# Kernel tuning notes

Measured on AMD Instinct MI355X. Metric: run time of the kernel, lower is better.

The kernel has to match this reference:

```python
import jax, jax.numpy as jnp
import numpy as np

BATCH = 32
NUM_PRIORS = 8732
NUM_CLASSES = 81          # includes background class 0
CENTER_VAR = 0.1
SIZE_VAR = 0.2
CONF_THR = 0.01
NMS_THR = 0.45
TOPK = 100                # per-class NMS candidates
MAX_DET = 100             # max detections per image


def setup_inputs() -> dict:
    key = jax.random.key(0)
    k1, k2, k3 = jax.random.split(key, 3)
    cls_logits = jax.random.normal(k1, (BATCH, NUM_PRIORS, NUM_CLASSES), jnp.float32)
    bbox_pred = jax.random.normal(k2, (BATCH, NUM_PRIORS, 4), jnp.float32)
    # center-form priors (cx, cy, w, h) in (0, 1)
    priors = jax.random.uniform(k3, (NUM_PRIORS, 4), jnp.float32, 0.05, 0.95)
    return {"cls_logits": cls_logits, "bbox_pred": bbox_pred, "priors": priors}


def _decode(loc, priors):
    # convert_locations_to_boxes (center form) then center_form_to_corner_form
    cxcy = loc[..., :2] * CENTER_VAR * priors[..., 2:] + priors[..., :2]
    wh = jnp.exp(loc[..., 2:] * SIZE_VAR) * priors[..., 2:]
    return jnp.concatenate([cxcy - wh * 0.5, cxcy + wh * 0.5], axis=-1)  # [.., 4] xyxy


def _pairwise_iou(b):
    # b: [K, 4] corner form
    lt = jnp.maximum(b[:, None, :2], b[None, :, :2])
    rb = jnp.minimum(b[:, None, 2:], b[None, :, 2:])
    wh = jnp.clip(rb - lt, 0.0)
    inter = wh[..., 0] * wh[..., 1]
    area = jnp.clip(b[:, 2] - b[:, 0], 0.0) * jnp.clip(b[:, 3] - b[:, 1], 0.0)
    return inter / (area[:, None] + area[None, :] - inter + 1e-9)


def _per_class_nms(scores_n, boxes_n):
    # scores_n: [N], boxes_n: [N, 4]
    s, idx = jax.lax.top_k(scores_n, TOPK)
    b = boxes_n[idx]                                # [K, 4]
    iou = _pairwise_iou(b)                          # [K, K]
    init = s > CONF_THR
    rng = jnp.arange(TOPK)

    def body(i, keep):
        sup = (iou[i] > NMS_THR) & keep[i] & (rng > i)
        return keep & ~sup

    keep = jax.lax.fori_loop(0, TOPK, body, init)   # greedy NMS on sorted boxes
    return jnp.where(keep, s, 0.0), b


def reference(cls_logits, bbox_pred, priors):
    scores = jax.nn.softmax(cls_logits, axis=-1)            # [B, N, C]
    boxes = _decode(bbox_pred, priors)                      # [B, N, 4]
    cls_scores = jnp.swapaxes(scores[..., 1:], 1, 2)        # [B, C-1, N] skip background
    nms_fn = jax.vmap(jax.vmap(_per_class_nms, in_axes=(0, None)), in_axes=(0, 0))
    s_k, b_k = nms_fn(cls_scores, boxes)                    # [B, C-1, K], [B, C-1, K, 4]
    labels = jnp.broadcast_to(jnp.arange(1, NUM_CLASSES)[None, :, None], s_k.shape)
    B = s_k.shape[0]
    flat = (NUM_CLASSES - 1) * TOPK
    s_f = s_k.reshape(B, flat)
    b_f = b_k.reshape(B, flat, 4)
    l_f = labels.reshape(B, flat)
    top_s, top_i = jax.lax.top_k(s_f, MAX_DET)              # keep best MAX_DET per image
    top_b = jnp.take_along_axis(b_f, top_i[..., None], axis=1)
    top_l = jnp.take_along_axis(l_f, top_i, axis=1)
    return top_b, top_s, top_l.astype(jnp.int32)
```

## Files before the change

kernel.cpp:

```cpp
#include <hip/hip_runtime.h>
#include <hip/hip_bf16.h>
#include <float.h>

#define BATCH    32
#define NPRIORS  8732
#define NT32     274
#define NPAD     (NT32 * 32)
#define NV4T     (NPAD / 4)
#define NCLASSES 81
#define NC1      80
#define TOPK     100
#define MAXDET   100
#define FLATC    (NC1 * TOPK)
#define FV4      2000
#define NCAND    512
#define NBIN     1024
#define BINOFF   3040

__global__ __launch_bounds__(256, 4) void softmax_transpose_kernel(
    const float* __restrict__ logits, float* __restrict__ scores_t) {
  int b = blockIdx.x / NT32;
  int tile = blockIdx.x - b * NT32;
  int n0 = tile * 32;
  int rows = min(32, NPRIORS - n0);

  int t = threadIdx.x;
  int r = t >> 3;
  int q = t & 7;

  __shared__ __align__(16) float lds[NC1 * 40];

  const bool live = (r < rows);

  float v[11];
  float s = 0.f;
  if (live) {
    const float* rowp = logits + ((size_t)b * NPRIORS + n0 + r) * NCLASSES;
#pragma unroll
    for (int k = 0; k < 10; ++k) v[k] = rowp[q + (k << 3)];
    v[10] = (q == 0) ? rowp[80] : -FLT_MAX;

    float m = -FLT_MAX;
#pragma unroll
    for (int k = 0; k < 10; ++k) m = fmaxf(m, v[k]);
    if (q == 0) m = fmaxf(m, v[10]);
    m = fmaxf(m, __shfl_xor(m, 1));
    m = fmaxf(m, __shfl_xor(m, 2));
    m = fmaxf(m, __shfl_xor(m, 4));

#pragma unroll
    for (int k = 0; k < 10; ++k) {
      v[k] = expf(v[k] - m);
      s += v[k];
    }
    if (q == 0) {
      v[10] = expf(v[10] - m);
      s += v[10];
    }
    s += __shfl_xor(s, 1);
    s += __shfl_xor(s, 2);
    s += __shfl_xor(s, 4);

#pragma unroll
    for (int k = 0; k < 10; ++k) {
      int c = q + (k << 3);
      if (c >= 1) lds[(c - 1) * 40 + r] = v[k] / s;
    }
    if (q == 0) lds[79 * 40 + r] = v[10] / s;
  } else {
#pragma unroll
    for (int k = 0; k < 10; ++k) {
      int c = q + (k << 3);
      if (c >= 1) lds[(c - 1) * 40 + r] = 0.f;
    }
    if (q == 0) lds[79 * 40 + r] = 0.f;
  }
  __syncthreads();

  float4* d4 = (float4*)(scores_t + (size_t)(b * NT32 + tile) * (NC1 * 32));
#pragma unroll
  for (int i = 0; i < 3; ++i) {
    int o4 = t + (i << 8);
    if (o4 < 640) {
      int c = o4 >> 3;
      int j = o4 & 7;
      d4[o4] = *(const float4*)&lds[c * 40 + (j << 2)];
    }
  }
}

__device__ __forceinline__ float4 decode_box(float4 l, float4 p) {
  float cx = l.x * 0.1f * p.z + p.x;
  float cy = l.y * 0.1f * p.w + p.y;
  float w  = expf(l.z * 0.2f) * p.z;
  float h  = expf(l.w * 0.2f) * p.w;
  return make_float4(cx - w * 0.5f, cy - h * 0.5f, cx + w * 0.5f,
                     cy + h * 0.5f);
}

__device__ __forceinline__ unsigned long long cex(unsigned long long key,
                                                  unsigned long long p,
                                                  bool up, bool low) {
  return (up == low) ? (key < p ? key : p) : (key > p ? key : p);
}

__global__ __launch_bounds__(256, 8) void topk_select_kernel(
    const float* __restrict__ scores_t, unsigned long long* __restrict__ k_sel) {
  const int bc = blockIdx.x;
  const int b = bc / NC1;
  const int c = bc - b * NC1;
  const int t = threadIdx.x;
  const int lane = t & 63;
  const int w = t >> 6;

  __shared__ __align__(16) unsigned int hist[NBIN * 2];
  __shared__ __align__(16) unsigned long long cand[NCAND];
  __shared__ int s_cnt, s_cut, wtot[4];

  const float4* s4 = (const float4*)scores_t;
  const size_t base4 = (size_t)b * (NT32 * NC1 * 8) + (size_t)c * 8;

  float va[36];
#pragma unroll
  for (int i = 0; i < 9; ++i) {
    int p = t + (i << 8);
    float4 v = make_float4(0.f, 0.f, 0.f, 0.f);
    if (p < NV4T) v = s4[base4 + (size_t)(p >> 3) * (NC1 * 8) + (p & 7)];
    va[4 * i + 0] = v.x; va[4 * i + 1] = v.y;
    va[4 * i + 2] = v.z; va[4 * i + 3] = v.w;
  }
#pragma unroll
  for (int j = 0; j < 36; ++j) asm volatile("" : "+v"(va[j]));

  uint4* h4 = (uint4*)hist;
  const uint4 z4 = make_uint4(0u, 0u, 0u, 0u);
  h4[t] = z4;
  h4[t + 256] = z4;
  cand[t] = ~0ull;
  cand[t + 256] = ~0ull;
  if (t == 0) { s_cnt = 0; s_cut = 0; }
  __syncthreads();

#pragma unroll
  for (int j = 0; j < 36; ++j) {
    unsigned int bits = __float_as_uint(va[j]);
    if (bits != 0u) {
      int bin = (int)(bits >> 18) - BINOFF;
      bin = max(0, min(NBIN - 1, bin));
      atomicAdd(&hist[(bin << 1) | (lane & 1)], 1u);
    }
  }
  __syncthreads();

  int h[4];
  int ls;
  {
    uint4 a = h4[2 * t];
    uint4 b2 = h4[2 * t + 1];
    h[0] = (int)(a.x + a.y);
    h[1] = (int)(a.z + a.w);
    h[2] = (int)(b2.x + b2.y);
    h[3] = (int)(b2.z + b2.w);
    ls = h[0] + h[1] + h[2] + h[3];
  }
  int s = ls;
#pragma unroll
  for (int off = 1; off < 64; off <<= 1) {
    int o = __shfl_down(s, off);
    if (lane + off < 64) s += o;
  }
  if (lane == 0) wtot[w] = s;
  __syncthreads();
  int upper = 0;
  for (int w2 = w + 1; w2 < 4; ++w2) upper += wtot[w2];
  int run = (s - ls) + upper;
  int cutbin = -1;
#pragma unroll
  for (int k = 3; k >= 0; --k) {
    if (run < TOPK && run + h[k] >= TOPK) cutbin = (t << 2) + k;
    run += h[k];
  }
  if (cutbin >= 0) s_cut = cutbin;
  __syncthreads();

  const unsigned int cutbits = (unsigned int)(s_cut + BINOFF) << 18;

  unsigned long long msk = 0ull;
  int cnt = 0;
#pragma unroll
  for (int j = 0; j < 36; ++j) {
    unsigned int bits = __float_as_uint(va[j]);
    if (bits >= cutbits) { msk |= 1ull << j; ++cnt; }
  }
  int inc = cnt;
#pragma unroll
  for (int off = 1; off < 64; off <<= 1) {
    int o = __shfl_up(inc, off);
    if (lane >= off) inc += o;
  }
  int wtotal = __shfl(inc, 63);
  int wbase = 0;
  if (lane == 63) wbase = atomicAdd(&s_cnt, wtotal);
  wbase = __shfl(wbase, 63);
  int pos = wbase + inc - cnt;
#pragma unroll
  for (int j = 0; j < 36; ++j) {
    if ((msk >> j) & 1ull) {
      if (pos < NCAND) {
        unsigned int bits = __float_as_uint(va[j]);
        int idx = ((t + ((j >> 2) << 8)) << 2) + (j & 3);
        cand[pos] = (((unsigned long long)(~bits)) << 32) | (unsigned int)idx;
      }
      ++pos;
    }
  }
  __syncthreads();

  const int ncand = s_cnt;
  if (ncand <= 256) {
    unsigned long long key = cand[t];
#pragma unroll
    for (int k2 = 2; k2 <= 256; k2 <<= 1) {
#pragma unroll
      for (int j = 128; j > 0; j >>= 1) {
        if (j >= k2) continue;
        const bool up = ((t & k2) == 0);
        if (j >= 64) {
          cand[t] = key;
          __syncthreads();
          unsigned long long p = cand[t ^ j];
          key = cex(key, p, up, (t & j) == 0);
          __syncthreads();
        } else {
          unsigned long long p = __shfl_xor(key, j);
          key = cex(key, p, up, (lane & j) == 0);
        }
      }
    }
    if (t < TOPK) k_sel[(size_t)bc * TOPK + t] = key;
  } else {
    int NS = 512;
    for (int k2 = 2; k2 <= NS; k2 <<= 1) {
      for (int j = k2 >> 1; j > 0; j >>= 1) {
        if (j >= 128) {
          __syncthreads();
          for (int p = t; p < NS; p += 256) {
            int ixj = p ^ j;
            if (ixj > p) {
              unsigned long long a = cand[p], c2 = cand[ixj];
              bool up = ((p & k2) == 0);
              if (up ? (a > c2) : (a < c2)) { cand[p] = c2; cand[ixj] = a; }
            }
          }
          __syncthreads();
        } else {
          int base = w << 7;
          if (base < NS) {
#pragma unroll
            for (int half = 0; half < 2; ++half) {
              int p = base + lane + (half << 6);
              int ixj = p ^ j;
              if (ixj > p) {
                unsigned long long a = cand[p], c2 = cand[ixj];
                bool up = ((p & k2) == 0);
                if (up ? (a > c2) : (a < c2)) { cand[p] = c2; cand[ixj] = a; }
              }
            }
          }
        }
      }
    }
    __syncthreads();
    if (t < TOPK) k_sel[(size_t)bc * TOPK + t] = cand[t];
  }
}

__global__ __launch_bounds__(256) void nms_kernel(
    const unsigned long long* __restrict__ k_sel,
    const float* __restrict__ loc, const float* __restrict__ priors,
    float* __restrict__ s_k, float* __restrict__ b_k) {
  const int t = threadIdx.x;
  const int lane = t & 63;
  const int w = t >> 6;
  const int bc = blockIdx.x;
  const int b = bc / NC1;

  __shared__ __align__(16) float4 lbox[TOPK];
  __shared__ float larea[TOPK];
  __shared__ float lscore[TOPK];
  __shared__ unsigned long long pm[4][64][3];
  __shared__ unsigned long long keepw[2];

  if (t < TOPK) {
    unsigned long long key = k_sel[(size_t)bc * TOPK + t];
    float sv = __uint_as_float(~(unsigned int)(key >> 32));
    int idx = (int)(key & 0xFFFFFFFFull);
    if ((unsigned)idx >= NPRIORS) { idx = 0; sv = 0.f; }
    float4 bx = decode_box(((const float4*)loc)[(size_t)b * NPRIORS + idx],
                           ((const float4*)priors)[idx]);
    lbox[t] = bx;
    larea[t] = fmaxf(bx.z - bx.x, 0.f) * fmaxf(bx.w - bx.y, 0.f);
    lscore[t] = sv;
  }
  __syncthreads();

  const bool hasb = (lane + 64) < TOPK;
  float4 ba = lbox[lane];
  float aa = larea[lane];
  float4 bb2 = lbox[hasb ? (lane + 64) : 0];
  float ab = larea[hasb ? (lane + 64) : 0];

  unsigned long long ra0 = 0, ra1 = 0, rb1 = 0;
  int jlo = max(1, w * 25);
  int jhi = min(TOPK, w * 25 + 25);
  for (int j = jlo; j < jhi; ++j) {
    float4 bj = lbox[j];
    float aj = larea[j];
    if (lane < j) {
      float iw = fmaxf(fminf(ba.z, bj.z) - fmaxf(ba.x, bj.x), 0.f);
      float ih = fmaxf(fminf(ba.w, bj.w) - fmaxf(ba.y, bj.y), 0.f);
      float inter = iw * ih;
      float iou = inter / (aa + aj - inter + 1e-9f);
      if (iou > 0.45f) {
        if (j < 64) ra0 |= 1ull << j; else ra1 |= 1ull << (j - 64);
      }
    }
    if (hasb && (lane + 64) < j) {
      float iw = fmaxf(fminf(bb2.z, bj.z) - fmaxf(bb2.x, bj.x), 0.f);
      float ih = fmaxf(fminf(bb2.w, bj.w) - fmaxf(bb2.y, bj.y), 0.f);
      float inter = iw * ih;
      float iou = inter / (ab + aj - inter + 1e-9f);
      if (iou > 0.45f) rb1 |= 1ull << (j - 64);
    }
  }
  pm[w][lane][0] = ra0;
  pm[w][lane][1] = ra1;
  pm[w][lane][2] = rb1;
  __syncthreads();

  if (w == 0) {
    unsigned long long fa0 = pm[0][lane][0] | pm[1][lane][0] |
                             pm[2][lane][0] | pm[3][lane][0];
    unsigned long long fa1 = pm[0][lane][1] | pm[1][lane][1] |
                             pm[2][lane][1] | pm[3][lane][1];
    unsigned long long fb1 = pm[0][lane][2] | pm[1][lane][2] |
                             pm[2][lane][2] | pm[3][lane][2];

    float sva = lscore[lane];
    float svb = hasb ? lscore[lane + 64] : 0.f;
    unsigned long long keep0 = __ballot(sva > 0.01f);
    unsigned long long keep1 = __ballot(hasb && (svb > 0.01f));
    for (int i = 0; i < TOPK; ++i) {
      bool il = i < 64;
      bool kb = il ? ((keep0 >> i) & 1ull) : ((keep1 >> (i - 64)) & 1ull);
      unsigned long long m0 = __shfl(il ? fa0 : 0ull, i & 63);
      unsigned long long m1 = __shfl(il ? fa1 : fb1, i & 63);
      if (kb) { keep0 &= ~m0; keep1 &= ~m1; }
    }
    if (lane == 0) { keepw[0] = keep0; keepw[1] = keep1; }
  }
  __syncthreads();

  if (t < TOPK) {
    bool kp = (t < 64) ? ((keepw[0] >> t) & 1ull)
                       : ((keepw[1] >> (t - 64)) & 1ull);
    s_k[(size_t)bc * TOPK + t] = kp ? lscore[t] : 0.f;
    ((float4*)(b_k + (size_t)bc * TOPK * 4))[t] = lbox[t];
  }
}

__global__ __launch_bounds__(256) void final_topk_kernel(
    const float* __restrict__ s_k, const float* __restrict__ b_k,
    float* __restrict__ out) {
  const int b = blockIdx.x;
  const int t = threadIdx.x;
  const int lane = t & 63;
  const int w = t >> 6;

  __shared__ __align__(16) unsigned int hist[NBIN * 2];
  __shared__ __align__(16) unsigned long long cand[NCAND];
  __shared__ int s_cnt, s_cut, wtot[4];

  const float4* src4 = (const float4*)(s_k + (size_t)b * FLATC);

  float va[32];
#pragma unroll
  for (int i = 0; i < 8; ++i) {
    int p = t + (i << 8);
    float4 v = make_float4(0.f, 0.f, 0.f, 0.f);
    if (p < FV4) v = src4[p];
    va[4 * i + 0] = v.x; va[4 * i + 1] = v.y;
    va[4 * i + 2] = v.z; va[4 * i + 3] = v.w;
  }

  uint4* h4 = (uint4*)hist;
  const uint4 z4 = make_uint4(0u, 0u, 0u, 0u);
  h4[t] = z4;
  h4[t + 256] = z4;
  cand[t] = ~0ull;
  cand[t + 256] = ~0ull;
  if (t == 0) { s_cnt = 0; s_cut = 0; }
  __syncthreads();

#pragma unroll
  for (int j = 0; j < 32; ++j) {
    unsigned int bits = __float_as_uint(va[j]);
    if (bits != 0u) {
      int bin = (int)(bits >> 18) - BINOFF;
      bin = max(0, min(NBIN - 1, bin));
      atomicAdd(&hist[(bin << 1) | (lane & 1)], 1u);
    }
  }
  __syncthreads();

  int h[4];
  int ls;
  {
    uint4 a = h4[2 * t];
    uint4 b2 = h4[2 * t + 1];
    h[0] = (int)(a.x + a.y);
    h[1] = (int)(a.z + a.w);
    h[2] = (int)(b2.x + b2.y);
    h[3] = (int)(b2.z + b2.w);
    ls = h[0] + h[1] + h[2] + h[3];
  }
  int s = ls;
#pragma unroll
  for (int off = 1; off < 64; off <<= 1) {
    int o = __shfl_down(s, off);
    if (lane + off < 64) s += o;
  }
  if (lane == 0) wtot[w] = s;
  __syncthreads();
  int upper = 0;
  for (int w2 = w + 1; w2 < 4; ++w2) upper += wtot[w2];
  int run = (s - ls) + upper;
  int cutbin = -1;
#pragma unroll
  for (int k = 3; k >= 0; --k) {
    if (run < TOPK && run + h[k] >= TOPK) cutbin = (t << 2) + k;
    run += h[k];
  }
  if (cutbin >= 0) s_cut = cutbin;
  __syncthreads();

  const unsigned int cutbits = (unsigned int)(s_cut + BINOFF) << 18;

  unsigned int msk = 0u;
  int cnt = 0;
#pragma unroll
  for (int j = 0; j < 32; ++j) {
    unsigned int bits = __float_as_uint(va[j]);
    if (bits >= cutbits) { msk |= 1u << j; ++cnt; }
  }
  int inc = cnt;
#pragma unroll
  for (int off = 1; off < 64; off <<= 1) {
    int o = __shfl_up(inc, off);
    if (lane >= off) inc += o;
  }
  int wtotal = __shfl(inc, 63);
  int wbase = 0;
  if (lane == 63) wbase = atomicAdd(&s_cnt, wtotal);
  wbase = __shfl(wbase, 63);
  int pos = wbase + inc - cnt;
#pragma unroll
  for (int j = 0; j < 32; ++j) {
    if ((msk >> j) & 1u) {
      if (pos < NCAND) {
        unsigned int bits = __float_as_uint(va[j]);
        int idx = ((t + ((j >> 2) << 8)) << 2) + (j & 3);
        cand[pos] = (((unsigned long long)(~bits)) << 32) | (unsigned int)idx;
      }
      ++pos;
    }
  }
  __syncthreads();

  const int ncand = s_cnt;
  unsigned long long okey;
  if (ncand <= 256) {
    unsigned long long key = cand[t];
#pragma unroll
    for (int k2 = 2; k2 <= 256; k2 <<= 1) {
#pragma unroll
      for (int j = 128; j > 0; j >>= 1) {
        if (j >= k2) continue;
        const bool up = ((t & k2) == 0);
        if (j >= 64) {
          cand[t] = key;
          __syncthreads();
          unsigned long long p = cand[t ^ j];
          key = cex(key, p, up, (t & j) == 0);
          __syncthreads();
        } else {
          unsigned long long p = __shfl_xor(key, j);
          key = cex(key, p, up, (lane & j) == 0);
        }
      }
    }
    okey = key;
  } else {
    int NS = 512;
    for (int k2 = 2; k2 <= NS; k2 <<= 1) {
      for (int j = k2 >> 1; j > 0; j >>= 1) {
        if (j >= 128) {
          __syncthreads();
          for (int p = t; p < NS; p += 256) {
            int ixj = p ^ j;
            if (ixj > p) {
              unsigned long long a = cand[p], c2 = cand[ixj];
              bool up = ((p & k2) == 0);
              if (up ? (a > c2) : (a < c2)) { cand[p] = c2; cand[ixj] = a; }
            }
          }
          __syncthreads();
        } else {
          int base = w << 7;
          if (base < NS) {
#pragma unroll
            for (int half = 0; half < 2; ++half) {
              int p = base + lane + (half << 6);
              int ixj = p ^ j;
              if (ixj > p) {
                unsigned long long a = cand[p], c2 = cand[ixj];
                bool up = ((p & k2) == 0);
                if (up ? (a > c2) : (a < c2)) { cand[p] = c2; cand[ixj] = a; }
              }
            }
          }
        }
      }
    }
    __syncthreads();
    okey = cand[min(t, NCAND - 1)];
  }

  if (t < MAXDET) {
    unsigned long long key = okey;
    unsigned int vb = ~(unsigned int)(key >> 32);
    float sv = __uint_as_float(vb);
    int f = (int)(key & 0xFFFFFFFFull);
    if ((unsigned)f >= FLATC) { f = 0; sv = 0.f; }
    float4 bb = *(const float4*)(b_k + ((size_t)b * FLATC + f) * 4);
    ((float4*)out)[b * MAXDET + t] = bb;
    out[BATCH * MAXDET * 4 + b * MAXDET + t] = sv;
    int cls = f / TOPK + 1;
    out[BATCH * MAXDET * 5 + b * MAXDET + t] = (float)cls;
  }
}

extern "C" void kernel_launch(void* const* d_in, const int* in_sizes, int n_in,
                              void* d_out, int out_size, void* d_ws,
                              size_t ws_size, hipStream_t stream) {
  const float* cls_logits = (const float*)d_in[0];
  const float* bbox_pred  = (const float*)d_in[1];
  const float* priors     = (const float*)d_in[2];
  float* out = (float*)d_out;

  float* scores_t = (float*)d_ws;
  float* s_k = scores_t + (size_t)BATCH * NT32 * NC1 * 32;
  float* b_k = s_k + (size_t)BATCH * NC1 * TOPK;
  unsigned long long* k_sel =
      (unsigned long long*)(b_k + (size_t)BATCH * NC1 * TOPK * 4);

  softmax_transpose_kernel<<<BATCH * NT32, 256, 0, stream>>>(cls_logits,
                                                             scores_t);
  topk_select_kernel<<<BATCH * NC1, 256, 0, stream>>>(scores_t, k_sel);
  nms_kernel<<<BATCH * NC1, 256, 0, stream>>>(k_sel, bbox_pred, priors,
                                              s_k, b_k);
  final_topk_kernel<<<BATCH, 256, 0, stream>>>(s_k, b_k, out);
}
```

Measured before the change: 105.5 us.

## Store transposed scores as 16-bit keys and recompute exact scores for candidates

The softmax kernel now writes only the upper 16 bits of each class score (a truncated float key) in the transposed layout, plus per-prior softmax max and sum stats. The top-k select kernel builds its histogram and threshold from these half-size keys. It then recomputes exact scores only for the surviving candidates by re-reading the logits and applying the stored stats. This halves the intermediate write and read traffic, at the cost of scattered logit gathers per candidate and coarser keys that may admit more candidates near the cutoff.

```diff
diff --git a/kernel.cpp b/kernel.cpp
--- a/kernel.cpp
+++ b/kernel.cpp
@@ -6,7 +6,6 @@
 #define NPRIORS  8732
 #define NT32     274
 #define NPAD     (NT32 * 32)
-#define NV4T     (NPAD / 4)
 #define NCLASSES 81
 #define NC1      80
 #define TOPK     100
@@ -16,9 +15,11 @@
 #define NCAND    512
 #define NBIN     1024
 #define BINOFF   3040
-
-__global__ __launch_bounds__(256, 4) void softmax_transpose_kernel(
-    const float* __restrict__ logits, float* __restrict__ scores_t) {
+#define NK4      (NT32 * 4)
+
+__global__ __launch_bounds__(256, 4) void softmax_stats_kernel(
+    const float* __restrict__ logits, unsigned short* __restrict__ key16,
+    float2* __restrict__ stats) {
   int b = blockIdx.x / NT32;
   int tile = blockIdx.x - b * NT32;
   int n0 = tile * 32;
@@ -28,14 +29,14 @@
   int r = t >> 3;
   int q = t & 7;
 
-  __shared__ __align__(16) float lds[NC1 * 40];
+  __shared__ __align__(16) unsigned int ldsu[NC1 * 16];
 
   const bool live = (r < rows);
 
-  float v[11];
-  float s = 0.f;
+  unsigned int out16[10];
   if (live) {
     const float* rowp = logits + ((size_t)b * NPRIORS + n0 + r) * NCLASSES;
+    float v[11];
 #pragma unroll
     for (int k = 0; k < 10; ++k) v[k] = rowp[q + (k << 3)];
     v[10] = (q == 0) ? rowp[80] : -FLT_MAX;
@@ -48,6 +49,7 @@
     m = fmaxf(m, __shfl_xor(m, 2));
     m = fmaxf(m, __shfl_xor(m, 4));
 
+    float s = 0.f;
 #pragma unroll
     for (int k = 0; k < 10; ++k) {
       v[k] = expf(v[k] - m);
@@ -63,30 +65,28 @@
 
 #pragma unroll
     for (int k = 0; k < 10; ++k) {
-      int c = q + (k << 3);
-      if (c >= 1) lds[(c - 1) * 40 + r] = v[k] / s;
-    }
-    if (q == 0) lds[79 * 40 + r] = v[10] / s;
+      float sc = v[k] / s;
+      out16[k] = __float_as_uint(sc) >> 16;
+    }
+    if (q == 0) out16[0] = __float_as_uint(v[10] / s) >> 16;
+    if (q == 0) stats[(size_t)b * NPAD + n0 + r] = make_float2(m, s);
   } else {
 #pragma unroll
-    for (int k = 0; k < 10; ++k) {
-      int c = q + (k << 3);
-      if (c >= 1) lds[(c - 1) * 40 + r] = 0.f;
-    }
-    if (q == 0) lds[79 * 40 + r] = 0.f;
-  }
-  __syncthreads();
-
-  float4* d4 = (float4*)(scores_t + (size_t)(b * NT32 + tile) * (NC1 * 32));
-#pragma unroll
-  for (int i = 0; i < 3; ++i) {
-    int o4 = t + (i << 8);
-    if (o4 < 640) {
-      int c = o4 >> 3;
-      int j = o4 & 7;
-      d4[o4] = *(const float4*)&lds[c * 40 + (j << 2)];
-    }
-  }
+    for (int k = 0; k < 10; ++k) out16[k] = 0u;
+  }
+
+#pragma unroll
+  for (int k = 0; k < 10; ++k) {
+    unsigned int part = (unsigned int)__shfl_xor((int)out16[k], 8);
+    if ((r & 1) == 0) {
+      int cls = (q == 0) ? ((k == 0) ? 79 : (8 * k - 1)) : (q - 1 + 8 * k);
+      ldsu[cls * 16 + (r >> 1)] = out16[k] | (part << 16);
+    }
+  }
+  __syncthreads();
+
+  uint4* dst = (uint4*)(key16 + (size_t)(b * NT32 + tile) * (NC1 * 32));
+  for (int i = t; i < 320; i += 256) dst[i] = ((const uint4*)ldsu)[i];
 }
 
 __device__ __forceinline__ float4 decode_box(float4 l, float4 p) {
@@ -105,7 +105,9 @@
 }
 
 __global__ __launch_bounds__(256, 8) void topk_select_kernel(
-    const float* __restrict__ scores_t, unsigned long long* __restrict__ k_sel) {
+    const unsigned short* __restrict__ key16,
+    const float* __restrict__ logits, const float2* __restrict__ stats,
+    unsigned long long* __restrict__ k_sel) {
   const int bc = blockIdx.x;
   const int b = bc / NC1;
   const int c = bc - b * NC1;
@@ -115,39 +117,49 @@
 
   __shared__ __align__(16) unsigned int hist[NBIN * 2];
   __shared__ __align__(16) unsigned long long cand[NCAND];
+  __shared__ __align__(16) unsigned int cidx[NCAND];
   __shared__ int s_cnt, s_cut, wtot[4];
 
-  const float4* s4 = (const float4*)scores_t;
-  const size_t base4 = (size_t)b * (NT32 * NC1 * 8) + (size_t)c * 8;
-
-  float va[36];
-#pragma unroll
-  for (int i = 0; i < 9; ++i) {
-    int p = t + (i << 8);
-    float4 v = make_float4(0.f, 0.f, 0.f, 0.f);
-    if (p < NV4T) v = s4[base4 + (size_t)(p >> 3) * (NC1 * 8) + (p & 7)];
-    va[4 * i + 0] = v.x; va[4 * i + 1] = v.y;
-    va[4 * i + 2] = v.z; va[4 * i + 3] = v.w;
-  }
-#pragma unroll
-  for (int j = 0; j < 36; ++j) asm volatile("" : "+v"(va[j]));
+  const uint4* k4 = (const uint4*)key16;
+  const size_t base4 = (size_t)b * (NT32 * NC1 * 4) + (size_t)c * 4;
+
+  uint4 va4[5];
+#pragma unroll
+  for (int i = 0; i < 5; ++i) {
+    int p4 = t + (i << 8);
+    uint4 v = make_uint4(0u, 0u, 0u, 0u);
+    if (p4 < NK4) v = k4[base4 + (size_t)(p4 >> 2) * (NC1 * 4) + (p4 & 3)];
+    va4[i] = v;
+  }
+#pragma unroll
+  for (int i = 0; i < 5; ++i)
+    asm volatile("" : "+v"(va4[i].x), "+v"(va4[i].y), "+v"(va4[i].z),
+                      "+v"(va4[i].w));
 
   uint4* h4 = (uint4*)hist;
   const uint4 z4 = make_uint4(0u, 0u, 0u, 0u);
   h4[t] = z4;
   h4[t + 256] = z4;
-  cand[t] = ~0ull;
-  cand[t + 256] = ~0ull;
   if (t == 0) { s_cnt = 0; s_cut = 0; }
   __syncthreads();
 
 #pragma unroll
-  for (int j = 0; j < 36; ++j) {
-    unsigned int bits = __float_as_uint(va[j]);
-    if (bits != 0u) {
-      int bin = (int)(bits >> 18) - BINOFF;
-      bin = max(0, min(NBIN - 1, bin));
-      atomicAdd(&hist[(bin << 1) | (lane & 1)], 1u);
+  for (int i = 0; i < 5; ++i) {
+    const unsigned int* cp = (const unsigned int*)&va4[i];
+#pragma unroll
+    for (int u = 0; u < 4; ++u) {
+      unsigned int cc = cp[u];
+      unsigned int lo = cc & 0xFFFFu, hi = cc >> 16;
+      if (lo) {
+        int bin = (int)(lo >> 2) - BINOFF;
+        bin = max(0, min(NBIN - 1, bin));
+        atomicAdd(&hist[(bin << 1) | (lane & 1)], 1u);
+      }
+      if (hi) {
+        int bin = (int)(hi >> 2) - BINOFF;
+        bin = max(0, min(NBIN - 1, bin));
+        atomicAdd(&hist[(bin << 1) | (lane & 1)], 1u);
+      }
     }
   }
   __syncthreads();
@@ -183,14 +195,19 @@
   if (cutbin >= 0) s_cut = cutbin;
   __syncthreads();
 
-  const unsigned int cutbits = (unsigned int)(s_cut + BINOFF) << 18;
+  const unsigned int cutk = (unsigned int)(s_cut + BINOFF) << 2;
 
   unsigned long long msk = 0ull;
   int cnt = 0;
 #pragma unroll
-  for (int j = 0; j < 36; ++j) {
-    unsigned int bits = __float_as_uint(va[j]);
-    if (bits >= cutbits) { msk |= 1ull << j; ++cnt; }
+  for (int i = 0; i < 5; ++i) {
+    const unsigned int* cp = (const unsigned int*)&va4[i];
+#pragma unroll
+    for (int u = 0; u < 4; ++u) {
+      unsigned int cc = cp[u];
+      if ((cc & 0xFFFFu) >= cutk) { msk |= 1ull << (i * 8 + u * 2); ++cnt; }
+      if ((cc >> 16) >= cutk)     { msk |= 1ull << (i * 8 + u * 2 + 1); ++cnt; }
+    }
   }
   int inc = cnt;
 #pragma unroll
@@ -204,21 +221,32 @@
   wbase = __shfl(wbase, 63);
   int pos = wbase + inc - cnt;
 #pragma unroll
-  for (int j = 0; j < 36; ++j) {
-    if ((msk >> j) & 1ull) {
-      if (pos < NCAND) {
-        unsigned int bits = __float_as_uint(va[j]);
-        int idx = ((t + ((j >> 2) << 8)) << 2) + (j & 3);
-        cand[pos] = (((unsigned long long)(~bits)) << 32) | (unsigned int)idx;
-      }
-      ++pos;
-    }
-  }
-  __syncthreads();
-
-  const int ncand = s_cnt;
+  for (int i = 0; i < 5; ++i) {
+    int p4 = t + (i << 8);
+    int bpr = ((p4 >> 2) << 5) + ((p4 & 3) << 3);
+#pragma unroll
+    for (int j = 0; j < 8; ++j) {
+      if ((msk >> (i * 8 + j)) & 1ull) {
+        if (pos < NCAND) cidx[pos] = (unsigned int)(bpr + j);
+        ++pos;
+      }
+    }
+  }
+  __syncthreads();
+
+  const int ncand = min(s_cnt, NCAND);
+
+  unsigned long long key = ~0ull;
+  if (t < ncand) {
+    int p = (int)cidx[t];
+    float l = logits[((size_t)b * NPRIORS + p) * NCLASSES + (c + 1)];
+    float2 st = stats[(size_t)b * NPAD + p];
+    float sc = expf(l - st.x) / st.y;
+    key = (((unsigned long long)(~__float_as_uint(sc))) << 32) |
+          (unsigned int)p;
+  }
+
   if (ncand <= 256) {
-    unsigned long long key = cand[t];
 #pragma unroll
     for (int k2 = 2; k2 <= 256; k2 <<= 1) {
 #pragma unroll
@@ -239,6 +267,18 @@
     }
     if (t < TOPK) k_sel[(size_t)bc * TOPK + t] = key;
   } else {
+    unsigned long long key2 = ~0ull;
+    if (t + 256 < ncand) {
+      int p = (int)cidx[t + 256];
+      float l = logits[((size_t)b * NPRIORS + p) * NCLASSES + (c + 1)];
+      float2 st = stats[(size_t)b * NPAD + p];
+      float sc = expf(l - st.x) / st.y;
+      key2 = (((unsigned long long)(~__float_as_uint(sc))) << 32) |
+             (unsigned int)p;
+    }
+    cand[t] = key;
+    cand[t + 256] = key2;
+    __syncthreads();
     int NS = 512;
     for (int k2 = 2; k2 <= NS; k2 <<= 1) {
       for (int j = k2 >> 1; j > 0; j >>= 1) {
@@ -558,15 +598,18 @@
   const float* priors     = (const float*)d_in[2];
   float* out = (float*)d_out;
 
-  float* scores_t = (float*)d_ws;
-  float* s_k = scores_t + (size_t)BATCH * NT32 * NC1 * 32;
+  unsigned short* key16 = (unsigned short*)d_ws;
+  const size_t key16_bytes = (size_t)BATCH * NT32 * NC1 * 32 * 2;
+  float2* stats = (float2*)((char*)d_ws + key16_bytes);
+  float* s_k = (float*)((char*)stats + (size_t)BATCH * NPAD * sizeof(float2));
   float* b_k = s_k + (size_t)BATCH * NC1 * TOPK;
   unsigned long long* k_sel =
       (unsigned long long*)(b_k + (size_t)BATCH * NC1 * TOPK * 4);
 
-  softmax_transpose_kernel<<<BATCH * NT32, 256, 0, stream>>>(cls_logits,
-                                                             scores_t);
-  topk_select_kernel<<<BATCH * NC1, 256, 0, stream>>>(scores_t, k_sel);
+  softmax_stats_kernel<<<BATCH * NT32, 256, 0, stream>>>(cls_logits, key16,
+                                                         stats);
+  topk_select_kernel<<<BATCH * NC1, 256, 0, stream>>>(key16, cls_logits,
+                                                      stats, k_sel);
   nms_kernel<<<BATCH * NC1, 256, 0, stream>>>(k_sel, bbox_pred, priors,
                                               s_k, b_k);
   final_topk_kernel<<<BATCH, 256, 0, stream>>>(s_k, b_k, out);
```

Result: no change. 106.4 us (+0.8%).
